# Performance work log

Hardware: AMD Instinct MI355X
Metric: run time of the kernel (lower is better)

## Reference

```python
import jax, jax.numpy as jnp
import numpy as np

D_MODEL = 1024
NUM_HEADS = 16
DEPTH = D_MODEL // NUM_HEADS
NEG_BIG = -1e9


def setup_inputs() -> dict:
    key = jax.random.key(0)
    ks = jax.random.split(key, 12)
    B, S = 2, 2048
    scale = 1.0 / np.sqrt(D_MODEL)
    inp = {
        "v": jax.random.normal(ks[0], (B, S, D_MODEL), jnp.float32),
        "k": jax.random.normal(ks[1], (B, S, D_MODEL), jnp.float32),
        "q": jax.random.normal(ks[2], (B, S, D_MODEL), jnp.float32),
        "mask": jnp.zeros((B, 1, 1, S), jnp.float32),
        "Wq": jax.random.normal(ks[3], (D_MODEL, D_MODEL), jnp.float32) * scale,
        "bq": jnp.zeros((D_MODEL,), jnp.float32),
        "Wk": jax.random.normal(ks[4], (D_MODEL, D_MODEL), jnp.float32) * scale,
        "bk": jnp.zeros((D_MODEL,), jnp.float32),
        "Wv": jax.random.normal(ks[5], (D_MODEL, D_MODEL), jnp.float32) * scale,
        "bv": jnp.zeros((D_MODEL,), jnp.float32),
        "Wo": jax.random.normal(ks[6], (D_MODEL, D_MODEL), jnp.float32) * scale,
        "bo": jnp.zeros((D_MODEL,), jnp.float32),
    }
    return inp


def _split_heads(x):
    # (B, S, D) -> (B, H, S, depth)
    B, S, _ = x.shape
    return x.reshape(B, S, NUM_HEADS, DEPTH).transpose(0, 2, 1, 3)


def reference(v, k, q, mask, Wq, bq, Wk, bk, Wv, bv, Wo, bo):
    B, S, _ = q.shape
    qh = _split_heads(q @ Wq + bq)  # (B,H,Sq,depth)
    kh = _split_heads(k @ Wk + bk)  # (B,H,Sk,depth)
    vh = _split_heads(v @ Wv + bv)  # (B,H,Sk,depth)

    logits = jnp.einsum("bhqd,bhkd->bhqk", qh, kh) / jnp.sqrt(
        jnp.asarray(DEPTH, jnp.float32))
    logits = logits + mask * NEG_BIG  # mask broadcasts over heads/queries
    attn = jax.nn.softmax(logits, axis=-1)  # (B,H,Sq,Sk)
    ctx = jnp.einsum("bhqk,bhkd->bhqd", attn, vh)
    ctx = ctx.transpose(0, 2, 1, 3).reshape(B, S, D_MODEL)
    out = ctx @ Wo + bo
    return out, attn
```

## Files before the change

kernel.cpp:

```cpp
#include <hip/hip_runtime.h>
#include <stdint.h>

#define S_LEN 2048
#define DMODEL 1024
#define NHEAD 16
#define DHEAD 64
#define NBATCH 2
#define NE 4194304
#define WN 1048576

typedef unsigned short u16;
typedef float f32x16 __attribute__((ext_vector_type(16)));
typedef __bf16 bf16x8 __attribute__((ext_vector_type(8)));

__device__ __forceinline__ u16 f2bf(float x) {
  union { float f; unsigned u; } v; v.f = x;
  unsigned r = v.u + 0x7fffu + ((v.u >> 16) & 1u);
  return (u16)(r >> 16);
}
__device__ __forceinline__ unsigned cvt_pk_bf16(float lo, float hi) {
  unsigned r;
  asm("v_cvt_pk_bf16_f32 %0, %1, %2" : "=v"(r) : "v"(lo), "v"(hi));
  return r;
}
__device__ __forceinline__ void gld_lds16(const void* g, void* l) {
  __builtin_amdgcn_global_load_lds(
      (const __attribute__((address_space(1))) unsigned*)g,
      (__attribute__((address_space(3))) unsigned*)l, 16, 0, 0);
}

__global__ __launch_bounds__(256) void cvt_inputs(
    const float* __restrict__ q, const float* __restrict__ k, const float* __restrict__ v,
    u16* __restrict__ xq, u16* __restrict__ xk, u16* __restrict__ xv)
{
  int i = blockIdx.x * 256 + threadIdx.x;
  const int stride = gridDim.x * 256;
  for (; i < NE / 4; i += stride) {
    float4 a = ((const float4*)q)[i];
    float4 b = ((const float4*)k)[i];
    float4 c = ((const float4*)v)[i];
    ushort4 oa, ob, oc;
    oa.x = f2bf(a.x); oa.y = f2bf(a.y); oa.z = f2bf(a.z); oa.w = f2bf(a.w);
    ob.x = f2bf(b.x); ob.y = f2bf(b.y); ob.z = f2bf(b.z); ob.w = f2bf(b.w);
    oc.x = f2bf(c.x); oc.y = f2bf(c.y); oc.z = f2bf(c.z); oc.w = f2bf(c.w);
    ((ushort4*)xq)[i] = oa;
    ((ushort4*)xk)[i] = ob;
    ((ushort4*)xv)[i] = oc;
  }
}

__global__ __launch_bounds__(256) void wtrans(
    const float* __restrict__ Wq, const float* __restrict__ Wk,
    const float* __restrict__ Wv, const float* __restrict__ Wo,
    u16* __restrict__ oq, u16* __restrict__ ok, u16* __restrict__ ov, u16* __restrict__ oo)
{
  __shared__ u16 t[64][65];
  const float* W; u16* O;
  if (blockIdx.z == 0)      { W = Wq; O = oq; }
  else if (blockIdx.z == 1) { W = Wk; O = ok; }
  else if (blockIdx.z == 2) { W = Wv; O = ov; }
  else                      { W = Wo; O = oo; }
  const int tid = threadIdx.x;
  const int r0 = blockIdx.y * 64, c0 = blockIdx.x * 64;
#pragma unroll
  for (int i = 0; i < 4; ++i) {
    const int row = i * 16 + (tid >> 4);
    const int col = (tid & 15) * 4;
    float4 wv = *(const float4*)(W + (size_t)(r0 + row) * DMODEL + c0 + col);
    t[row][col + 0] = f2bf(wv.x);
    t[row][col + 1] = f2bf(wv.y);
    t[row][col + 2] = f2bf(wv.z);
    t[row][col + 3] = f2bf(wv.w);
  }
  __syncthreads();
#pragma unroll
  for (int i = 0; i < 4; ++i) {
    const int row = i * 16 + (tid >> 4);
    const int col = (tid & 15) * 4;
    ushort4 o;
    o.x = t[col + 0][row]; o.y = t[col + 1][row];
    o.z = t[col + 2][row]; o.w = t[col + 3][row];
    *(ushort4*)(O + (size_t)(c0 + row) * DMODEL + r0 + col) = o;
  }
}

template <int OUTMODE>
__device__ __forceinline__ void gemm_core(
    const u16* __restrict__ A, const u16* __restrict__ Bt,
    const float* __restrict__ bias, void* __restrict__ outp,
    float scale, int m0, int n0)
{
  __shared__ u16 As[128 * 32];
  __shared__ u16 Bs[128 * 32];
  const int tid = threadIdx.x;
  const int lane = tid & 63, w = tid >> 6;
  const int q_l = lane & 31, hi = lane >> 5;
  const int wr = w >> 1, wc = w & 1;

  f32x16 acc[2][2];
#pragma unroll
  for (int a = 0; a < 2; ++a)
#pragma unroll
    for (int b = 0; b < 2; ++b)
#pragma unroll
      for (int r = 0; r < 16; ++r) acc[a][b][r] = 0.f;

  const u16* srcA = A + (size_t)(m0 + (tid >> 2)) * DMODEL + (tid & 3) * 8;
  const u16* srcB = Bt + (size_t)(n0 + (tid >> 2)) * DMODEL + (tid & 3) * 8;
  u16* dstA = As + w * 512;
  u16* dstB = Bs + w * 512;

  for (int kt = 0; kt < DMODEL; kt += 32) {
    gld_lds16(srcA + kt, dstA);
    gld_lds16(srcA + kt + (size_t)64 * DMODEL, dstA + 2048);
    gld_lds16(srcB + kt, dstB);
    gld_lds16(srcB + kt + (size_t)64 * DMODEL, dstB + 2048);
    __syncthreads();
#pragma unroll
    for (int kk = 0; kk < 2; ++kk) {
      bf16x8 af[2], bfv[2];
#pragma unroll
      for (int mb = 0; mb < 2; ++mb)
        af[mb] = *reinterpret_cast<const bf16x8*>(&As[(wr * 64 + mb * 32 + q_l) * 32 + kk * 16 + hi * 8]);
#pragma unroll
      for (int nb = 0; nb < 2; ++nb)
        bfv[nb] = *reinterpret_cast<const bf16x8*>(&Bs[(wc * 64 + nb * 32 + q_l) * 32 + kk * 16 + hi * 8]);
#pragma unroll
      for (int mb = 0; mb < 2; ++mb)
#pragma unroll
        for (int nb = 0; nb < 2; ++nb)
          acc[mb][nb] = __builtin_amdgcn_mfma_f32_32x32x16_bf16(af[mb], bfv[nb], acc[mb][nb], 0, 0, 0);
    }
    __syncthreads();
  }

#pragma unroll
  for (int mb = 0; mb < 2; ++mb) {
#pragma unroll
    for (int nb = 0; nb < 2; ++nb) {
      const int n = n0 + wc * 64 + nb * 32 + q_l;
      const float bn = bias[n];
#pragma unroll
      for (int r = 0; r < 16; ++r) {
        const int m = m0 + wr * 64 + mb * 32 + (r & 3) + 8 * (r >> 2) + 4 * hi;
        const float val = (acc[mb][nb][r] + bn) * scale;
        if (OUTMODE == 0) {
          const int bb = m >> 11, s = m & 2047, hh = n >> 6, d = n & 63;
          ((u16*)outp)[(((size_t)(bb * NHEAD + hh)) * S_LEN + s) * DHEAD + d] = f2bf(val);
        } else {
          ((float*)outp)[(size_t)m * DMODEL + n] = val;
        }
      }
    }
  }
}

__global__ __launch_bounds__(256) void gemm_qkv(
    const u16* __restrict__ xq, const u16* __restrict__ xk, const u16* __restrict__ xv,
    const u16* __restrict__ wqt, const u16* __restrict__ wkt, const u16* __restrict__ wvt,
    const float* __restrict__ bq, const float* __restrict__ bk, const float* __restrict__ bv,
    u16* __restrict__ qh, u16* __restrict__ kh, u16* __restrict__ vh)
{
  const u16 *A, *Bt; const float* bias; u16* O; float scale;
  if (blockIdx.z == 0)      { A = xq; Bt = wqt; bias = bq; O = qh; scale = 0.125f; }
  else if (blockIdx.z == 1) { A = xk; Bt = wkt; bias = bk; O = kh; scale = 1.f; }
  else                      { A = xv; Bt = wvt; bias = bv; O = vh; scale = 1.f; }
  gemm_core<0>(A, Bt, bias, O, scale, blockIdx.y * 128, blockIdx.x * 128);
}

__global__ __launch_bounds__(256) void vtrans(const u16* __restrict__ vh, u16* __restrict__ vt)
{
  __shared__ u16 t[64][72];
  const int tid = threadIdx.x;
  const int id = blockIdx.x;
  const int h = ((id & 7) << 1) | ((id >> 3) & 1);
  const int b = (id >> 4) & 1;
  const int bh = b * 16 + h;
  const int s0 = (id >> 5) * 64;
  const u16* src = vh + (size_t)bh * S_LEN * DHEAD;
  u16* dst = vt + (size_t)bh * DHEAD * S_LEN;
#pragma unroll
  for (int i = 0; i < 2; ++i) {
    const int row = i * 32 + (tid >> 3);
    const int c8 = (tid & 7) * 8;
    *(uint4*)&t[row][c8] = *(const uint4*)(src + (size_t)(s0 + row) * DHEAD + c8);
  }
  __syncthreads();
#pragma unroll
  for (int i = 0; i < 2; ++i) {
    const int d = i * 32 + (tid >> 3);
    const int c8 = (tid & 7) * 8;
    unsigned p0 = (unsigned)t[c8 + 0][d] | ((unsigned)t[c8 + 1][d] << 16);
    unsigned p1 = (unsigned)t[c8 + 2][d] | ((unsigned)t[c8 + 3][d] << 16);
    unsigned p2 = (unsigned)t[c8 + 4][d] | ((unsigned)t[c8 + 5][d] << 16);
    unsigned p3 = (unsigned)t[c8 + 6][d] | ((unsigned)t[c8 + 7][d] << 16);
    uint4 o; o.x = p0; o.y = p1; o.z = p2; o.w = p3;
    *(uint4*)(dst + (size_t)d * S_LEN + s0 + c8) = o;
  }
}

__global__ __launch_bounds__(64, 2) void attn_pv(
    const u16* __restrict__ qh, const u16* __restrict__ kh,
    const u16* __restrict__ vt, const float* __restrict__ mask,
    float* __restrict__ inv_g, u16* __restrict__ ctx_out)
{
  const int lane = threadIdx.x;
  const int q_l = lane & 31, hi = lane >> 5;
  const int id = blockIdx.x;
  const int h = ((id & 7) << 1) | ((id >> 3) & 1);
  const int b = (id >> 4) & 1;
  const int bh = b * 16 + h;
  const int qb = id >> 5;
  const int q0 = qb * 64;

  const u16* Qp = qh + (size_t)bh * S_LEN * DHEAD;
  const u16* Kp = kh + (size_t)bh * S_LEN * DHEAD;
  const u16* Vp = vt + (size_t)bh * DHEAD * S_LEN;
  const float* mrow = mask + (size_t)b * S_LEN;

  bf16x8 qfA[4], qfB[4];
  {
    const u16* qrA = Qp + (size_t)(q0 + q_l) * DHEAD + hi * 8;
    const u16* qrB = Qp + (size_t)(q0 + 32 + q_l) * DHEAD + hi * 8;
#pragma unroll
    for (int c = 0; c < 4; ++c) {
      qfA[c] = *reinterpret_cast<const bf16x8*>(qrA + c * 16);
      qfB[c] = *reinterpret_cast<const bf16x8*>(qrB + c * 16);
    }
  }

  float rsumA = 0.f, rsumB = 0.f;
  f32x16 caccA[2], caccB[2];
#pragma unroll
  for (int db = 0; db < 2; ++db)
#pragma unroll
    for (int r = 0; r < 16; ++r) { caccA[db][r] = 0.f; caccB[db][r] = 0.f; }

  bf16x8 kc[4], kn[4], vc[2][2], vn[2][2];
  {
    const u16* kr0 = Kp + (size_t)q_l * DHEAD + hi * 8;
#pragma unroll
    for (int c = 0; c < 4; ++c) kc[c] = *reinterpret_cast<const bf16x8*>(kr0 + c * 16);
#pragma unroll
    for (int s2 = 0; s2 < 2; ++s2)
#pragma unroll
      for (int db = 0; db < 2; ++db)
        vc[s2][db] = *reinterpret_cast<const bf16x8*>(
            Vp + (size_t)(db * 32 + q_l) * S_LEN + s2 * 16 + hi * 8);
  }

#pragma unroll 1
  for (int t = 0; t < 64; ++t) {
    const int k0 = t * 32;
    if (t < 63) {
      const u16* krow = Kp + (size_t)(k0 + 32 + q_l) * DHEAD + hi * 8;
#pragma unroll
      for (int c = 0; c < 4; ++c) kn[c] = *reinterpret_cast<const bf16x8*>(krow + c * 16);
#pragma unroll
      for (int s2 = 0; s2 < 2; ++s2)
#pragma unroll
        for (int db = 0; db < 2; ++db)
          vn[s2][db] = *reinterpret_cast<const bf16x8*>(
              Vp + (size_t)(db * 32 + q_l) * S_LEN + k0 + 32 + s2 * 16 + hi * 8);
    }
    {
      f32x16 a0, a1;
#pragma unroll
      for (int r = 0; r < 16; ++r) { a0[r] = 0.f; a1[r] = 0.f; }
      a0 = __builtin_amdgcn_mfma_f32_32x32x16_bf16(kc[0], qfA[0], a0, 0, 0, 0);
      a0 = __builtin_amdgcn_mfma_f32_32x32x16_bf16(kc[1], qfA[1], a0, 0, 0, 0);
      a1 = __builtin_amdgcn_mfma_f32_32x32x16_bf16(kc[2], qfA[2], a1, 0, 0, 0);
      a1 = __builtin_amdgcn_mfma_f32_32x32x16_bf16(kc[3], qfA[3], a1, 0, 0, 0);
      float p[16];
#pragma unroll
      for (int g = 0; g < 4; ++g) {
        const float4 mk = *(const float4*)&mrow[k0 + 8 * g + 4 * hi];
        p[4 * g + 0] = __expf(a0[4 * g + 0] + a1[4 * g + 0] + mk.x * -1e9f);
        p[4 * g + 1] = __expf(a0[4 * g + 1] + a1[4 * g + 1] + mk.y * -1e9f);
        p[4 * g + 2] = __expf(a0[4 * g + 2] + a1[4 * g + 2] + mk.z * -1e9f);
        p[4 * g + 3] = __expf(a0[4 * g + 3] + a1[4 * g + 3] + mk.w * -1e9f);
        rsumA += (p[4 * g + 0] + p[4 * g + 1]) + (p[4 * g + 2] + p[4 * g + 3]);
      }
      unsigned pk[8];
#pragma unroll
      for (int g = 0; g < 4; ++g) {
        pk[2 * g + 0] = cvt_pk_bf16(p[4 * g + 0], p[4 * g + 1]);
        pk[2 * g + 1] = cvt_pk_bf16(p[4 * g + 2], p[4 * g + 3]);
      }
#pragma unroll
      for (int s2 = 0; s2 < 2; ++s2) {
        unsigned x0 = pk[4 * s2 + 0], y0 = pk[4 * s2 + 2];
        unsigned x1 = pk[4 * s2 + 1], y1 = pk[4 * s2 + 3];
        asm volatile("v_permlane32_swap_b32 %0, %1" : "+v"(x0), "+v"(y0));
        asm volatile("v_permlane32_swap_b32 %0, %1" : "+v"(x1), "+v"(y1));
        uint4 fr; fr.x = x0; fr.y = x1; fr.z = y0; fr.w = y1;
        bf16x8 pa = __builtin_bit_cast(bf16x8, fr);
#pragma unroll
        for (int db = 0; db < 2; ++db)
          caccA[db] = __builtin_amdgcn_mfma_f32_32x32x16_bf16(pa, vc[s2][db], caccA[db], 0, 0, 0);
      }
    }
    {
      f32x16 a0, a1;
#pragma unroll
      for (int r = 0; r < 16; ++r) { a0[r] = 0.f; a1[r] = 0.f; }
      a0 = __builtin_amdgcn_mfma_f32_32x32x16_bf16(kc[0], qfB[0], a0, 0, 0, 0);
      a0 = __builtin_amdgcn_mfma_f32_32x32x16_bf16(kc[1], qfB[1], a0, 0, 0, 0);
      a1 = __builtin_amdgcn_mfma_f32_32x32x16_bf16(kc[2], qfB[2], a1, 0, 0, 0);
      a1 = __builtin_amdgcn_mfma_f32_32x32x16_bf16(kc[3], qfB[3], a1, 0, 0, 0);
      float p[16];
#pragma unroll
      for (int g = 0; g < 4; ++g) {
        const float4 mk = *(const float4*)&mrow[k0 + 8 * g + 4 * hi];
        p[4 * g + 0] = __expf(a0[4 * g + 0] + a1[4 * g + 0] + mk.x * -1e9f);
        p[4 * g + 1] = __expf(a0[4 * g + 1] + a1[4 * g + 1] + mk.y * -1e9f);
        p[4 * g + 2] = __expf(a0[4 * g + 2] + a1[4 * g + 2] + mk.z * -1e9f);
        p[4 * g + 3] = __expf(a0[4 * g + 3] + a1[4 * g + 3] + mk.w * -1e9f);
        rsumB += (p[4 * g + 0] + p[4 * g + 1]) + (p[4 * g + 2] + p[4 * g + 3]);
      }
      unsigned pk[8];
#pragma unroll
      for (int g = 0; g < 4; ++g) {
        pk[2 * g + 0] = cvt_pk_bf16(p[4 * g + 0], p[4 * g + 1]);
        pk[2 * g + 1] = cvt_pk_bf16(p[4 * g + 2], p[4 * g + 3]);
      }
#pragma unroll
      for (int s2 = 0; s2 < 2; ++s2) {
        unsigned x0 = pk[4 * s2 + 0], y0 = pk[4 * s2 + 2];
        unsigned x1 = pk[4 * s2 + 1], y1 = pk[4 * s2 + 3];
        asm volatile("v_permlane32_swap_b32 %0, %1" : "+v"(x0), "+v"(y0));
        asm volatile("v_permlane32_swap_b32 %0, %1" : "+v"(x1), "+v"(y1));
        uint4 fr; fr.x = x0; fr.y = x1; fr.z = y0; fr.w = y1;
        bf16x8 pb = __builtin_bit_cast(bf16x8, fr);
#pragma unroll
        for (int db = 0; db < 2; ++db)
          caccB[db] = __builtin_amdgcn_mfma_f32_32x32x16_bf16(pb, vc[s2][db], caccB[db], 0, 0, 0);
      }
    }
#pragma unroll
    for (int c = 0; c < 4; ++c) kc[c] = kn[c];
#pragma unroll
    for (int s2 = 0; s2 < 2; ++s2)
#pragma unroll
      for (int db = 0; db < 2; ++db) vc[s2][db] = vn[s2][db];
  }

  rsumA += __shfl_xor(rsumA, 32, 64);
  rsumB += __shfl_xor(rsumB, 32, 64);
  const float invA = 1.0f / rsumA;
  const float invB = 1.0f / rsumB;
  if (lane < 32) {
    inv_g[(size_t)bh * S_LEN + q0 + lane] = invA;
    inv_g[(size_t)bh * S_LEN + q0 + 32 + lane] = invB;
  }

  float scA[16], scB[16];
#pragma unroll
  for (int r = 0; r < 16; ++r) {
    const int src = (r & 3) + 8 * (r >> 2) + 4 * hi;
    scA[r] = __shfl(invA, src, 64);
    scB[r] = __shfl(invB, src, 64);
  }
#pragma unroll
  for (int db = 0; db < 2; ++db)
#pragma unroll
    for (int r = 0; r < 16; ++r) {
      const int qq = (r & 3) + 8 * (r >> 2) + 4 * hi;
      ctx_out[((size_t)(b * S_LEN + q0 + qq)) * DMODEL + h * DHEAD + db * 32 + q_l] =
          f2bf(caccA[db][r] * scA[r]);
      ctx_out[((size_t)(b * S_LEN + q0 + 32 + qq)) * DMODEL + h * DHEAD + db * 32 + q_l] =
          f2bf(caccB[db][r] * scB[r]);
    }
}

__global__ __launch_bounds__(256) void tail_fused(
    const u16* __restrict__ ctx, const u16* __restrict__ wot, const float* __restrict__ bo,
    float* __restrict__ out,
    const u16* __restrict__ qh, const u16* __restrict__ kh,
    const float* __restrict__ mask, const float* __restrict__ inv_g,
    float* __restrict__ attn_out)
{
  if (blockIdx.x < 256) {
    const int gid = blockIdx.x;
    gemm_core<1>(ctx, wot, bo, out, 1.f, (gid >> 3) * 128, (gid & 7) * 128);
    return;
  }
  const int id = blockIdx.x - 256;
  const int tid = threadIdx.x;
  const int lane = tid & 63, w = tid >> 6;
  const int q_l = lane & 31, hi = lane >> 5;
  const int h = ((id & 7) << 1) | ((id >> 3) & 1);
  const int b = (id >> 4) & 1;
  const int bh = b * 16 + h;
  const int qb = id >> 5;
  const int q0 = qb * 64;

  const u16* Qp = qh + (size_t)bh * S_LEN * DHEAD;
  const u16* Kp = kh + (size_t)bh * S_LEN * DHEAD;

  bf16x8 qfA[4], qfB[4];
  {
    const u16* qrA = Qp + (size_t)(q0 + q_l) * DHEAD + hi * 8;
    const u16* qrB = Qp + (size_t)(q0 + 32 + q_l) * DHEAD + hi * 8;
#pragma unroll
    for (int c = 0; c < 4; ++c) {
      qfA[c] = *reinterpret_cast<const bf16x8*>(qrA + c * 16);
      qfB[c] = *reinterpret_cast<const bf16x8*>(qrB + c * 16);
    }
  }

  float myinvA[16], myinvB[16];
#pragma unroll
  for (int r = 0; r < 16; ++r) {
    const int rq = (r & 3) + 8 * (r >> 2) + 4 * hi;
    myinvA[r] = inv_g[(size_t)bh * S_LEN + q0 + rq];
    myinvB[r] = inv_g[(size_t)bh * S_LEN + q0 + 32 + rq];
  }

  const int k0w = w * 512;
  float mval[16];
#pragma unroll
  for (int t = 0; t < 16; ++t)
    mval[t] = mask[(size_t)b * S_LEN + k0w + t * 32 + q_l] * -1e9f;

  float* baseA = attn_out + ((size_t)bh * S_LEN + q0 + 4 * hi) * S_LEN + k0w + q_l;
  float* baseB = attn_out + ((size_t)bh * S_LEN + q0 + 32 + 4 * hi) * S_LEN + k0w + q_l;

  bf16x8 kc[4], kn[4];
  {
    const u16* kr0 = Kp + (size_t)(k0w + q_l) * DHEAD + hi * 8;
#pragma unroll
    for (int c = 0; c < 4; ++c) kc[c] = *reinterpret_cast<const bf16x8*>(kr0 + c * 16);
  }

#pragma unroll
  for (int t = 0; t < 16; ++t) {
    if (t < 15) {
      const u16* krow = Kp + (size_t)(k0w + (t + 1) * 32 + q_l) * DHEAD + hi * 8;
#pragma unroll
      for (int c = 0; c < 4; ++c) kn[c] = *reinterpret_cast<const bf16x8*>(krow + c * 16);
    }
    {
      f32x16 a0, a1;
#pragma unroll
      for (int r = 0; r < 16; ++r) { a0[r] = 0.f; a1[r] = 0.f; }
      a0 = __builtin_amdgcn_mfma_f32_32x32x16_bf16(qfA[0], kc[0], a0, 0, 0, 0);
      a0 = __builtin_amdgcn_mfma_f32_32x32x16_bf16(qfA[1], kc[1], a0, 0, 0, 0);
      a1 = __builtin_amdgcn_mfma_f32_32x32x16_bf16(qfA[2], kc[2], a1, 0, 0, 0);
      a1 = __builtin_amdgcn_mfma_f32_32x32x16_bf16(qfA[3], kc[3], a1, 0, 0, 0);
#pragma unroll
      for (int r = 0; r < 16; ++r) {
        const float pv = __expf(a0[r] + a1[r] + mval[t]) * myinvA[r];
        const int rr = (r & 3) + 8 * (r >> 2);
        baseA[(size_t)rr * S_LEN + t * 32] = pv;
      }
    }
    {
      f32x16 a0, a1;
#pragma unroll
      for (int r = 0; r < 16; ++r) { a0[r] = 0.f; a1[r] = 0.f; }
      a0 = __builtin_amdgcn_mfma_f32_32x32x16_bf16(qfB[0], kc[0], a0, 0, 0, 0);
      a0 = __builtin_amdgcn_mfma_f32_32x32x16_bf16(qfB[1], kc[1], a0, 0, 0, 0);
      a1 = __builtin_amdgcn_mfma_f32_32x32x16_bf16(qfB[2], kc[2], a1, 0, 0, 0);
      a1 = __builtin_amdgcn_mfma_f32_32x32x16_bf16(qfB[3], kc[3], a1, 0, 0, 0);
#pragma unroll
      for (int r = 0; r < 16; ++r) {
        const float pv = __expf(a0[r] + a1[r] + mval[t]) * myinvB[r];
        const int rr = (r & 3) + 8 * (r >> 2);
        baseB[(size_t)rr * S_LEN + t * 32] = pv;
      }
    }
#pragma unroll
    for (int c = 0; c < 4; ++c) kc[c] = kn[c];
  }
}

extern "C" void kernel_launch(void* const* d_in, const int* in_sizes, int n_in,
                              void* d_out, int out_size, void* d_ws, size_t ws_size,
                              hipStream_t stream)
{
  (void)in_sizes; (void)n_in; (void)out_size; (void)ws_size;
  const float* v    = (const float*)d_in[0];
  const float* k    = (const float*)d_in[1];
  const float* q    = (const float*)d_in[2];
  const float* mask = (const float*)d_in[3];
  const float* Wq   = (const float*)d_in[4];
  const float* bq   = (const float*)d_in[5];
  const float* Wk   = (const float*)d_in[6];
  const float* bk   = (const float*)d_in[7];
  const float* Wv   = (const float*)d_in[8];
  const float* bv   = (const float*)d_in[9];
  const float* Wo   = (const float*)d_in[10];
  const float* bo   = (const float*)d_in[11];

  u16* ws16 = (u16*)d_ws;
  u16* xq  = ws16;
  u16* xk  = ws16 + (size_t)1 * NE;
  u16* xv  = ws16 + (size_t)2 * NE;
  u16* qh  = ws16 + (size_t)3 * NE;
  u16* kh  = ws16 + (size_t)4 * NE;
  u16* vh  = ws16 + (size_t)5 * NE;
  u16* wqt = ws16 + (size_t)6 * NE;
  u16* wkt = wqt + WN;
  u16* wvt = wkt + WN;
  u16* wot = wvt + WN;
  float* inv_g = (float*)(wot + WN);
  u16* vt  = xq;
  u16* ctx = xk;

  float* outp  = (float*)d_out;
  float* attnp = outp + (size_t)NE;

  cvt_inputs<<<dim3(1024), dim3(256), 0, stream>>>(q, k, v, xq, xk, xv);
  wtrans<<<dim3(16, 16, 4), dim3(256), 0, stream>>>(Wq, Wk, Wv, Wo, wqt, wkt, wvt, wot);
  gemm_qkv<<<dim3(8, 32, 3), dim3(256), 0, stream>>>(xq, xk, xv, wqt, wkt, wvt,
                                                     bq, bk, bv, qh, kh, vh);
  vtrans<<<dim3(1024), dim3(256), 0, stream>>>(vh, vt);
  attn_pv<<<dim3(1024), dim3(64), 0, stream>>>(qh, kh, vt, mask, inv_g, ctx);
  tail_fused<<<dim3(1280), dim3(256), 0, stream>>>(ctx, wot, bo, outp,
                                                   qh, kh, mask, inv_g, attnp);
}
```

Baseline: 324.6 us.

## Process 128 query rows per attention-write block with nontemporal stores

The attention-probability part of the fused tail kernel now covers 128 query rows per block instead of 64. Each loaded K tile is reused across four query sub-tiles, and the grid shrinks from 1280 to 768 blocks. The attn stores become nontemporal to avoid polluting cache with the large write-once output. It also sets launch_bounds with 2 blocks per CU and stops unrolling the key loop, which risks register pressure and less parallelism from fewer blocks.

```diff
diff --git a/kernel.cpp b/kernel.cpp
--- a/kernel.cpp
+++ b/kernel.cpp
@@ -373,7 +373,7 @@
     }
 }
 
-__global__ __launch_bounds__(256) void tail_fused(
+__global__ __launch_bounds__(256, 2) void tail_fused(
     const u16* __restrict__ ctx, const u16* __restrict__ wot, const float* __restrict__ bo,
     float* __restrict__ out,
     const u16* __restrict__ qh, const u16* __restrict__ kh,
@@ -392,30 +392,29 @@
   const int h = ((id & 7) << 1) | ((id >> 3) & 1);
   const int b = (id >> 4) & 1;
   const int bh = b * 16 + h;
-  const int qb = id >> 5;
-  const int q0 = qb * 64;
+  const int qg = id >> 5;
+  const int q0 = qg * 128;
 
   const u16* Qp = qh + (size_t)bh * S_LEN * DHEAD;
   const u16* Kp = kh + (size_t)bh * S_LEN * DHEAD;
 
-  bf16x8 qfA[4], qfB[4];
-  {
-    const u16* qrA = Qp + (size_t)(q0 + q_l) * DHEAD + hi * 8;
-    const u16* qrB = Qp + (size_t)(q0 + 32 + q_l) * DHEAD + hi * 8;
-#pragma unroll
-    for (int c = 0; c < 4; ++c) {
-      qfA[c] = *reinterpret_cast<const bf16x8*>(qrA + c * 16);
-      qfB[c] = *reinterpret_cast<const bf16x8*>(qrB + c * 16);
-    }
-  }
-
-  float myinvA[16], myinvB[16];
-#pragma unroll
-  for (int r = 0; r < 16; ++r) {
-    const int rq = (r & 3) + 8 * (r >> 2) + 4 * hi;
-    myinvA[r] = inv_g[(size_t)bh * S_LEN + q0 + rq];
-    myinvB[r] = inv_g[(size_t)bh * S_LEN + q0 + 32 + rq];
-  }
+  bf16x8 qf[4][4];
+#pragma unroll
+  for (int s = 0; s < 4; ++s) {
+    const u16* qr = Qp + (size_t)(q0 + s * 32 + q_l) * DHEAD + hi * 8;
+#pragma unroll
+    for (int c = 0; c < 4; ++c)
+      qf[s][c] = *reinterpret_cast<const bf16x8*>(qr + c * 16);
+  }
+
+  float myinv[4][16];
+#pragma unroll
+  for (int s = 0; s < 4; ++s)
+#pragma unroll
+    for (int r = 0; r < 16; ++r) {
+      const int rq = (r & 3) + 8 * (r >> 2) + 4 * hi;
+      myinv[s][r] = inv_g[(size_t)bh * S_LEN + q0 + s * 32 + rq];
+    }
 
   const int k0w = w * 512;
   float mval[16];
@@ -423,8 +422,10 @@
   for (int t = 0; t < 16; ++t)
     mval[t] = mask[(size_t)b * S_LEN + k0w + t * 32 + q_l] * -1e9f;
 
-  float* baseA = attn_out + ((size_t)bh * S_LEN + q0 + 4 * hi) * S_LEN + k0w + q_l;
-  float* baseB = attn_out + ((size_t)bh * S_LEN + q0 + 32 + 4 * hi) * S_LEN + k0w + q_l;
+  float* base[4];
+#pragma unroll
+  for (int s = 0; s < 4; ++s)
+    base[s] = attn_out + ((size_t)bh * S_LEN + q0 + s * 32 + 4 * hi) * S_LEN + k0w + q_l;
 
   bf16x8 kc[4], kn[4];
   {
@@ -433,41 +434,27 @@
     for (int c = 0; c < 4; ++c) kc[c] = *reinterpret_cast<const bf16x8*>(kr0 + c * 16);
   }
 
-#pragma unroll
+#pragma unroll 1
   for (int t = 0; t < 16; ++t) {
     if (t < 15) {
       const u16* krow = Kp + (size_t)(k0w + (t + 1) * 32 + q_l) * DHEAD + hi * 8;
 #pragma unroll
       for (int c = 0; c < 4; ++c) kn[c] = *reinterpret_cast<const bf16x8*>(krow + c * 16);
     }
-    {
+#pragma unroll
+    for (int s = 0; s < 4; ++s) {
       f32x16 a0, a1;
 #pragma unroll
       for (int r = 0; r < 16; ++r) { a0[r] = 0.f; a1[r] = 0.f; }
-      a0 = __builtin_amdgcn_mfma_f32_32x32x16_bf16(qfA[0], kc[0], a0, 0, 0, 0);
-      a0 = __builtin_amdgcn_mfma_f32_32x32x16_bf16(qfA[1], kc[1], a0, 0, 0, 0);
-      a1 = __builtin_amdgcn_mfma_f32_32x32x16_bf16(qfA[2], kc[2], a1, 0, 0, 0);
-      a1 = __builtin_amdgcn_mfma_f32_32x32x16_bf16(qfA[3], kc[3], a1, 0, 0, 0);
+      a0 = __builtin_amdgcn_mfma_f32_32x32x16_bf16(qf[s][0], kc[0], a0, 0, 0, 0);
+      a0 = __builtin_amdgcn_mfma_f32_32x32x16_bf16(qf[s][1], kc[1], a0, 0, 0, 0);
+      a1 = __builtin_amdgcn_mfma_f32_32x32x16_bf16(qf[s][2], kc[2], a1, 0, 0, 0);
+      a1 = __builtin_amdgcn_mfma_f32_32x32x16_bf16(qf[s][3], kc[3], a1, 0, 0, 0);
 #pragma unroll
       for (int r = 0; r < 16; ++r) {
-        const float pv = __expf(a0[r] + a1[r] + mval[t]) * myinvA[r];
+        const float pv = __expf(a0[r] + a1[r] + mval[t]) * myinv[s][r];
         const int rr = (r & 3) + 8 * (r >> 2);
-        baseA[(size_t)rr * S_LEN + t * 32] = pv;
-      }
-    }
-    {
-      f32x16 a0, a1;
-#pragma unroll
-      for (int r = 0; r < 16; ++r) { a0[r] = 0.f; a1[r] = 0.f; }
-      a0 = __builtin_amdgcn_mfma_f32_32x32x16_bf16(qfB[0], kc[0], a0, 0, 0, 0);
-      a0 = __builtin_amdgcn_mfma_f32_32x32x16_bf16(qfB[1], kc[1], a0, 0, 0, 0);
-      a1 = __builtin_amdgcn_mfma_f32_32x32x16_bf16(qfB[2], kc[2], a1, 0, 0, 0);
-      a1 = __builtin_amdgcn_mfma_f32_32x32x16_bf16(qfB[3], kc[3], a1, 0, 0, 0);
-#pragma unroll
-      for (int r = 0; r < 16; ++r) {
-        const float pv = __expf(a0[r] + a1[r] + mval[t]) * myinvB[r];
-        const int rr = (r & 3) + 8 * (r >> 2);
-        baseB[(size_t)rr * S_LEN + t * 32] = pv;
+        __builtin_nontemporal_store(pv, &base[s][(size_t)rr * S_LEN + t * 32]);
       }
     }
 #pragma unroll
@@ -517,6 +504,6 @@
                                                      bq, bk, bv, qh, kh, vh);
   vtrans<<<dim3(1024), dim3(256), 0, stream>>>(vh, vt);
   attn_pv<<<dim3(1024), dim3(64), 0, stream>>>(qh, kh, vt, mask, inv_g, ctx);
-  tail_fused<<<dim3(1280), dim3(256), 0, stream>>>(ctx, wot, bo, outp,
-                                                   qh, kh, mask, inv_g, attnp);
-}
+  tail_fused<<<dim3(768), dim3(256), 0, stream>>>(ctx, wot, bo, outp,
+                                                  qh, kh, mask, inv_g, attnp);
+}
```

Measured after the change: 299.9 us. 1.08x faster.
